# Optimization experiments

Measured on AMD Instinct MI355X. Metric: run time of the kernel, lower is better.

The kernel has to match this reference:

```python
import jax, jax.numpy as jnp
import numpy as np
import math

D_MODEL = 1024
N_HEADS = 16
HEAD_DIM = D_MODEL // N_HEADS


def get_slopes(n_heads: int) -> jnp.ndarray:
    def pow2_slopes(n):
        start = 2.0 ** (-8.0 / n)
        return np.array([start * start ** i for i in range(n)], dtype=np.float32)
    if math.log2(n_heads).is_integer():
        return jnp.asarray(pow2_slopes(n_heads))
    closest = 2 ** math.floor(math.log2(n_heads))
    base = pow2_slopes(closest)
    extra = pow2_slopes(2 * closest)[::2][: n_heads - closest]
    return jnp.asarray(np.concatenate([base, extra]))


def setup_inputs() -> dict:
    key = jax.random.key(0)
    ks = jax.random.split(key, 9)
    s = 1.0 / math.sqrt(D_MODEL)
    x = jax.random.normal(ks[0], (2, 2048, D_MODEL), dtype=jnp.float32)
    q_w = jax.random.uniform(ks[1], (D_MODEL, D_MODEL), jnp.float32, -s, s)
    q_b = jax.random.uniform(ks[2], (D_MODEL,), jnp.float32, -s, s)
    k_w = jax.random.uniform(ks[3], (D_MODEL, D_MODEL), jnp.float32, -s, s)
    k_b = jax.random.uniform(ks[4], (D_MODEL,), jnp.float32, -s, s)
    v_w = jax.random.uniform(ks[5], (D_MODEL, D_MODEL), jnp.float32, -s, s)
    v_b = jax.random.uniform(ks[6], (D_MODEL,), jnp.float32, -s, s)
    o_w = jax.random.uniform(ks[7], (D_MODEL, D_MODEL), jnp.float32, -s, s)
    o_b = jax.random.uniform(ks[8], (D_MODEL,), jnp.float32, -s, s)
    return {"x": x, "q_w": q_w, "q_b": q_b, "k_w": k_w, "k_b": k_b,
            "v_w": v_w, "v_b": v_b, "o_w": o_w, "o_b": o_b}


def reference(x, q_w, q_b, k_w, k_b, v_w, v_b, o_w, o_b):
    B, S, D = x.shape
    H, hd = N_HEADS, HEAD_DIM
    # torch Linear: y = x @ W.T + b
    Q = (x @ q_w.T + q_b).reshape(B, S, H, hd).transpose(0, 2, 1, 3)  # [B,H,S,hd]
    K = (x @ k_w.T + k_b).reshape(B, S, H, hd).transpose(0, 2, 1, 3)
    V = (x @ v_w.T + v_b).reshape(B, S, H, hd).transpose(0, 2, 1, 3)
    scores = jnp.einsum('bhqd,bhkd->bhqk', Q, K) / math.sqrt(hd)
    # ALiBi bias: slopes[h] * (k_pos - q_pos)
    pos = jnp.arange(S)
    rel = (pos[None, :] - pos[:, None]).astype(scores.dtype)  # [S,S]
    slopes = get_slopes(H)
    scores = scores + slopes[None, :, None, None] * rel[None, None, :, :]
    # causal mask
    causal = pos[None, :] <= pos[:, None]  # [S,S] True where allowed
    scores = jnp.where(causal[None, None], scores, -jnp.inf)
    attn = jax.nn.softmax(scores, axis=-1)  # dropout=0 (eval)
    out = jnp.einsum('bhqk,bhkd->bhqd', attn, V)
    out = out.transpose(0, 2, 1, 3).reshape(B, S, D)
    return out @ o_w.T + o_b
```

## Files before the change

### kernel.cpp

```cpp
#include <hip/hip_runtime.h>
#include <hip/hip_bf16.h>

typedef __attribute__((ext_vector_type(8))) short short8;
typedef __attribute__((ext_vector_type(4))) float float4v;
typedef __attribute__((ext_vector_type(4))) short short4v;
typedef __attribute__((ext_vector_type(4))) unsigned int uint4v;
typedef __attribute__((ext_vector_type(2))) unsigned int uint2v;

#define B_ 2
#define S_ 2048
#define D_ 1024
#define H_ 16
#define HD_ 64
#define M_ 4096
#define LOG2E 1.442695040888963f

__device__ __forceinline__ unsigned short f2bf(float f) {
  unsigned int u = __builtin_bit_cast(unsigned int, f);
  u += 0x7fffu + ((u >> 16) & 1u);
  return (unsigned short)(u >> 16);
}

__device__ __forceinline__ unsigned int pkbf(float a, float b) {
  __hip_bfloat162 h = __float22bfloat162_rn(make_float2(a, b));
  unsigned int u;
  __builtin_memcpy(&u, &h, sizeof(u));
  return u;
}

__device__ __forceinline__ void gload_lds16(const void* g, void* l) {
  __builtin_amdgcn_global_load_lds(
      (const __attribute__((address_space(1))) void*)g,
      (__attribute__((address_space(3))) void*)l, 16, 0, 0);
}

__global__ __launch_bounds__(256, 4) void cvt_kernel(
    const float* __restrict__ x,  const float* __restrict__ qw,
    const float* __restrict__ kw, const float* __restrict__ vw,
    const float* __restrict__ ow, unsigned short* __restrict__ dst)
{
  const int seg = blockIdx.y;
  const float* src;
  size_t doff;
  if (seg < 4)       { src = x + (size_t)seg * 1048576; doff = (size_t)seg * 1048576; }
  else if (seg == 4) { src = qw; doff = 4194304u; }
  else if (seg == 5) { src = kw; doff = 4194304u + 1048576u; }
  else if (seg == 6) { src = vw; doff = 4194304u + 2097152u; }
  else               { src = ow; doff = 4194304u + 3145728u; }
  const size_t i = ((size_t)blockIdx.x * 256 + threadIdx.x) * 4;
  float4v v = *(const float4v*)(src + i);
  short4v p;
#pragma unroll
  for (int r = 0; r < 4; ++r) p[r] = (short)f2bf(v[r]);
  *(short4v*)(dst + doff + i) = p;
}

__global__ __launch_bounds__(256, 2) void gemm_kernel(
    const unsigned short* __restrict__ X,
    const unsigned short* __restrict__ W0, const unsigned short* __restrict__ W1,
    const unsigned short* __restrict__ W2,
    const float* __restrict__ Bi0, const float* __restrict__ Bi1,
    const float* __restrict__ Bi2,
    unsigned short* O0, unsigned short* O1, unsigned short* O2,
    float* OutF, int md0, int md1, int md2)
{
  const int z = blockIdx.z;
  const unsigned short* W  = (z == 0) ? W0  : ((z == 1) ? W1  : W2);
  const float* Bi          = (z == 0) ? Bi0 : ((z == 1) ? Bi1 : Bi2);
  unsigned short* Out      = (z == 0) ? O0  : ((z == 1) ? O1  : O2);
  const int mode           = (z == 0) ? md0 : ((z == 1) ? md1 : md2);

  __shared__ __align__(16) char smem[128 * 32 * 2 * 2];
  __shared__ __align__(16) float tb[32 * 132];
  char* As = smem;
  char* Bs = smem + 128 * 32 * 2;

  const int t = threadIdx.x, l = t & 63;
  const int w = t >> 6, lr = l & 15, lg = l >> 4;
  const int n0 = blockIdx.x * 128, m0 = blockIdx.y * 128;
  const int wm = (w >> 1) * 64, wn = (w & 1) * 64;

  float4v acc[4][4];
#pragma unroll
  for (int i = 0; i < 4; ++i)
#pragma unroll
    for (int j = 0; j < 4; ++j) acc[i][j] = (float4v){0.f, 0.f, 0.f, 0.f};

  const int c0 = t, c1 = t + 256;
  const int r0 = c0 >> 2, k80 = (c0 & 3) * 8;
  const int r1 = c1 >> 2, k81 = (c1 & 3) * 8;

  for (int k0 = 0; k0 < 1024; k0 += 32) {
    __syncthreads();
    gload_lds16(X + (size_t)(m0 + r0) * 1024 + k0 + k80, As + c0 * 16);
    gload_lds16(X + (size_t)(m0 + r1) * 1024 + k0 + k81, As + c1 * 16);
    gload_lds16(W + (size_t)(n0 + r0) * 1024 + k0 + k80, Bs + c0 * 16);
    gload_lds16(W + (size_t)(n0 + r1) * 1024 + k0 + k81, Bs + c1 * 16);
    __syncthreads();

    short8 af[4], bfr[4];
#pragma unroll
    for (int i = 0; i < 4; ++i)
      af[i] = *(const short8*)(As + (wm + i * 16 + lr) * 64 + lg * 16);
#pragma unroll
    for (int j = 0; j < 4; ++j)
      bfr[j] = *(const short8*)(Bs + (wn + j * 16 + lr) * 64 + lg * 16);
#pragma unroll
    for (int i = 0; i < 4; ++i)
#pragma unroll
      for (int j = 0; j < 4; ++j)
        acc[i][j] = __builtin_amdgcn_mfma_f32_16x16x32_bf16(af[i], bfr[j], acc[i][j], 0, 0, 0);
  }

  float bv[4];
#pragma unroll
  for (int j = 0; j < 4; ++j) bv[j] = Bi[n0 + wn + j * 16 + lr];

  if (mode == 1) {
    const int rbase = (w >> 1) * 16;
    const int row16 = t >> 3, chunk = t & 7;
#pragma unroll
    for (int i = 0; i < 4; ++i) {
#pragma unroll
      for (int j = 0; j < 4; ++j)
#pragma unroll
        for (int r = 0; r < 4; ++r)
          tb[(rbase + lg * 4 + r) * 132 + wn + j * 16 + lr] = acc[i][j][r] + bv[j];
      __syncthreads();
      const int grow = m0 + ((row16 < 16) ? (i * 16 + row16) : (64 + i * 16 + row16 - 16));
      const int b = grow >> 11, sl = grow & 2047;
      const int colg = n0 + chunk * 16;
      const int hh = colg >> 6, d0 = colg & 63;
      float4v v4[4];
#pragma unroll
      for (int q = 0; q < 4; ++q)
        v4[q] = *(const float4v*)(tb + row16 * 132 + chunk * 16 + q * 4);
      uint4v lo, hi;
#pragma unroll
      for (int q = 0; q < 2; ++q) {
        lo[q * 2]     = pkbf(v4[q][0], v4[q][1]);
        lo[q * 2 + 1] = pkbf(v4[q][2], v4[q][3]);
        hi[q * 2]     = pkbf(v4[q + 2][0], v4[q + 2][1]);
        hi[q * 2 + 1] = pkbf(v4[q + 2][2], v4[q + 2][3]);
      }
      unsigned short* dst = Out + ((size_t)(b * H_ + hh) * S_ + sl) * HD_ + d0;
      *(short8*)dst = __builtin_bit_cast(short8, lo);
      *(short8*)(dst + 8) = __builtin_bit_cast(short8, hi);
      __syncthreads();
    }
  } else {
#pragma unroll
    for (int i = 0; i < 4; ++i) {
      const int rowb = m0 + wm + i * 16 + lg * 4;
#pragma unroll
      for (int j = 0; j < 4; ++j) {
        const int col = n0 + wn + j * 16 + lr;
        if (mode == 2) {
          const int b = rowb >> 11, s = rowb & 2047;
          const int hh = col >> 6, d = col & 63;
          uint2v pk2;
          pk2[0] = pkbf(acc[i][j][0] + bv[j], acc[i][j][1] + bv[j]);
          pk2[1] = pkbf(acc[i][j][2] + bv[j], acc[i][j][3] + bv[j]);
          *(short4v*)(Out + ((size_t)(b * H_ + hh) * HD_ + d) * S_ + s) =
              __builtin_bit_cast(short4v, pk2);
        } else {
#pragma unroll
          for (int r = 0; r < 4; ++r)
            OutF[(size_t)(rowb + r) * 1024 + col] = acc[i][j][r] + bv[j];
        }
      }
    }
  }
}

__global__ __launch_bounds__(256, 2) void attn_kernel(
    const unsigned short* __restrict__ Q, const unsigned short* __restrict__ K,
    const unsigned short* __restrict__ VT, unsigned short* __restrict__ O)
{
  __shared__ __align__(16) char smem[32768];

  const int t = threadIdx.x, l = t & 63;
  const int w = t >> 6, lr = l & 15, lg = l >> 4;
  const int bh = blockIdx.x;
  const int it = 31 - (int)blockIdx.y;
  const int h = bh & 15;

  const unsigned short* qbp = Q + (size_t)bh * S_ * HD_;
  const unsigned short* kbp = K + (size_t)bh * S_ * HD_;
  const unsigned short* vbp = VT + (size_t)bh * HD_ * S_;

  const float slope2 = __builtin_amdgcn_exp2f(-0.5f * (float)(h + 1)) * LOG2E;
  const float qksc = 0.125f * LOG2E;

  const int g0 = t, g1 = t + 256;
  const int sr0 = g0 >> 3, sc0 = (g0 & 7) ^ (sr0 & 7);
  const int sr1 = g1 >> 3, sc1 = (g1 & 7) ^ (sr1 & 7);

  const int fchunk = ((4 + lg) ^ (lr & 7)) * 16;
  const int fchunk0 = ((lg) ^ (lr & 7)) * 16;

  const int qrow = it * 64 + w * 16;
  const int qpos = qrow + lr;

  float kb16[4][4];
#pragma unroll
  for (int nj = 0; nj < 4; ++nj)
#pragma unroll
    for (int r = 0; r < 4; ++r)
      kb16[nj][r] = slope2 * (float)(nj * 16 + lg * 4 + r);

  short8 qf[2];
#pragma unroll
  for (int ks = 0; ks < 2; ++ks)
    qf[ks] = *(const short8*)(qbp + (size_t)(qrow + lr) * HD_ + ks * 32 + lg * 8);

  float4v o_acc[4];
#pragma unroll
  for (int dt = 0; dt < 4; ++dt) o_acc[dt] = (float4v){0.f, 0.f, 0.f, 0.f};
  float m_st = -1e30f, l_st = 0.f;

  gload_lds16(kbp + (size_t)sr0 * HD_ + sc0 * 8, smem + g0 * 16);
  gload_lds16(kbp + (size_t)sr1 * HD_ + sc1 * 8, smem + g1 * 16);
  gload_lds16(vbp + (size_t)sr0 * S_ + sc0 * 8, smem + 16384 + g0 * 16);
  gload_lds16(vbp + (size_t)sr1 * S_ + sc1 * 8, smem + 16384 + g1 * 16);
  __syncthreads();

  for (int j = 0; j <= it; ++j) {
    const int cur = j & 1;
    char* Ks = smem + (cur ? 8192 : 0);
    char* Vs = smem + 16384 + (cur ? 8192 : 0);
    if (j < it) {
      char* Kn = smem + (cur ? 0 : 8192);
      char* Vn = smem + 16384 + (cur ? 0 : 8192);
      const int jn = j + 1;
      gload_lds16(kbp + (size_t)(jn * 64 + sr0) * HD_ + sc0 * 8, Kn + g0 * 16);
      gload_lds16(kbp + (size_t)(jn * 64 + sr1) * HD_ + sc1 * 8, Kn + g1 * 16);
      gload_lds16(vbp + (size_t)sr0 * S_ + jn * 64 + sc0 * 8, Vn + g0 * 16);
      gload_lds16(vbp + (size_t)sr1 * S_ + jn * 64 + sc1 * 8, Vn + g1 * 16);
    }

    float4v s_acc[4];
#pragma unroll
    for (int nj = 0; nj < 4; ++nj) {
      s_acc[nj] = (float4v){0.f, 0.f, 0.f, 0.f};
      short8 kf0 = *(const short8*)(Ks + (nj * 16 + lr) * 128 + fchunk0);
      s_acc[nj] = __builtin_amdgcn_mfma_f32_16x16x32_bf16(kf0, qf[0], s_acc[nj], 0, 0, 0);
      short8 kf1 = *(const short8*)(Ks + (nj * 16 + lr) * 128 + fchunk);
      s_acc[nj] = __builtin_amdgcn_mfma_f32_16x16x32_bf16(kf1, qf[1], s_acc[nj], 0, 0, 0);
    }

    const float cj = slope2 * (float)(j * 64);
#pragma unroll
    for (int nj = 0; nj < 4; ++nj)
#pragma unroll
      for (int r = 0; r < 4; ++r)
        s_acc[nj][r] = s_acc[nj][r] * qksc + (cj + kb16[nj][r]);
    if (j == it) {
#pragma unroll
      for (int nj = 0; nj < 4; ++nj)
#pragma unroll
        for (int r = 0; r < 4; ++r) {
          const int kpos = j * 64 + nj * 16 + lg * 4 + r;
          if (kpos > qpos) s_acc[nj][r] = -1e30f;
        }
    }

    float mx = s_acc[0][0];
#pragma unroll
    for (int nj = 0; nj < 4; ++nj)
#pragma unroll
      for (int r = 0; r < 4; ++r) mx = fmaxf(mx, s_acc[nj][r]);
    mx = fmaxf(mx, __shfl_xor(mx, 16, 64));
    mx = fmaxf(mx, __shfl_xor(mx, 32, 64));
    const float mn = fmaxf(m_st, mx);
    const float alpha = __builtin_amdgcn_exp2f(m_st - mn);
    m_st = mn;
    float rsum = 0.f;
#pragma unroll
    for (int nj = 0; nj < 4; ++nj)
#pragma unroll
      for (int r = 0; r < 4; ++r) {
        const float p = __builtin_amdgcn_exp2f(s_acc[nj][r] - mn);
        s_acc[nj][r] = p;
        rsum += p;
      }
    rsum += __shfl_xor(rsum, 16, 64);
    rsum += __shfl_xor(rsum, 32, 64);
    l_st = alpha * l_st + rsum;
#pragma unroll
    for (int dt = 0; dt < 4; ++dt)
#pragma unroll
      for (int r = 0; r < 4; ++r) o_acc[dt][r] *= alpha;

    short8 pT[2];
#pragma unroll
    for (int njp = 0; njp < 2; ++njp) {
      uint4v u;
      u[0] = pkbf(s_acc[njp * 2][0], s_acc[njp * 2][1]);
      u[1] = pkbf(s_acc[njp * 2][2], s_acc[njp * 2][3]);
      u[2] = pkbf(s_acc[njp * 2 + 1][0], s_acc[njp * 2 + 1][1]);
      u[3] = pkbf(s_acc[njp * 2 + 1][2], s_acc[njp * 2 + 1][3]);
      pT[njp] = __builtin_bit_cast(short8, u);
    }

    const int vcl = lr & 7;
#pragma unroll
    for (int dt = 0; dt < 4; ++dt) {
      const char* rowp = Vs + (dt * 16 + lr) * 128;
#pragma unroll
      for (int njp = 0; njp < 2; ++njp) {
        const int cA = ((njp * 4 + (lg >> 1)) ^ vcl) * 16 + (lg & 1) * 8;
        const int cB = ((njp * 4 + 2 + (lg >> 1)) ^ vcl) * 16 + (lg & 1) * 8;
        short4v v0 = *(const short4v*)(rowp + cA);
        short4v v1 = *(const short4v*)(rowp + cB);
        short8 vf8;
#pragma unroll
        for (int e = 0; e < 4; ++e) { vf8[e] = v0[e]; vf8[e + 4] = v1[e]; }
        o_acc[dt] = __builtin_amdgcn_mfma_f32_16x16x32_bf16(vf8, pT[njp], o_acc[dt], 0, 0, 0);
      }
    }
    __syncthreads();
  }

  char* tw = smem + w * 4416;
#pragma unroll
  for (int dt = 0; dt < 4; ++dt)
#pragma unroll
    for (int r = 0; r < 4; ++r)
      *(float*)(tw + ((dt * 16 + lg * 4 + r) * 17 + lr) * 4) = o_acc[dt][r];
  if (lg == 0) *(float*)(tw + 4352 + lr * 4) = l_st;

  const int q2 = l >> 2, dbase = (l & 3) * 16;
  const float invl = 1.0f / *(const float*)(tw + 4352 + q2 * 4);
  uint4v os0, os1;
#pragma unroll
  for (int k = 0; k < 8; ++k) {
    const float va = *(const float*)(tw + ((dbase + 2 * k) * 17 + q2) * 4) * invl;
    const float vb = *(const float*)(tw + ((dbase + 2 * k + 1) * 17 + q2) * 4) * invl;
    if (k < 4) os0[k] = pkbf(va, vb); else os1[k - 4] = pkbf(va, vb);
  }
  const int brow = (bh >> 4) * S_;
  unsigned short* op = O + (size_t)(brow + qrow + q2) * 1024 + h * 64 + dbase;
  *(short8*)op = __builtin_bit_cast(short8, os0);
  *(short8*)(op + 8) = __builtin_bit_cast(short8, os1);
}

extern "C" void kernel_launch(void* const* d_in, const int* in_sizes, int n_in,
                              void* d_out, int out_size, void* d_ws, size_t ws_size,
                              hipStream_t stream) {
  (void)in_sizes; (void)n_in; (void)out_size; (void)ws_size;
  const float* x  = (const float*)d_in[0];
  const float* qw = (const float*)d_in[1];
  const float* qb = (const float*)d_in[2];
  const float* kw = (const float*)d_in[3];
  const float* kb = (const float*)d_in[4];
  const float* vw = (const float*)d_in[5];
  const float* vb = (const float*)d_in[6];
  const float* ow = (const float*)d_in[7];
  const float* ob = (const float*)d_in[8];
  float* out = (float*)d_out;

  unsigned short* xb  = (unsigned short*)d_ws;
  unsigned short* qwb = xb  + (size_t)M_ * D_;
  unsigned short* kwb = qwb + (size_t)D_ * D_;
  unsigned short* vwb = kwb + (size_t)D_ * D_;
  unsigned short* owb = vwb + (size_t)D_ * D_;
  unsigned short* qws = owb + (size_t)D_ * D_;
  unsigned short* kws = qws + (size_t)M_ * D_;
  unsigned short* vws = kws + (size_t)M_ * D_;
  unsigned short* aws = vws + (size_t)M_ * D_;

  cvt_kernel<<<dim3(1024, 8), dim3(256), 0, stream>>>(x, qw, kw, vw, ow, xb);
  gemm_kernel<<<dim3(8, 32, 3), dim3(256), 0, stream>>>(
      xb, qwb, kwb, vwb, qb, kb, vb, qws, kws, vws, out, 1, 1, 2);
  attn_kernel<<<dim3(32, 32), dim3(256), 0, stream>>>(qws, kws, vws, aws);
  gemm_kernel<<<dim3(8, 32, 1), dim3(256), 0, stream>>>(
      aws, owb, owb, owb, ob, ob, ob, aws, aws, aws, out, 0, 0, 0);
}
```

Before: 194.4 us.

## Use narrower output-projection GEMM tiles and compute softmax row sums via MFMA

Templates the GEMM on the N tile width and launches the output projection with 64-wide tiles, doubling block count from 256 to 512 so more CUs are filled. In attention, the softmax denominator is accumulated by an MFMA against a ones vector over the bf16 probabilities, replacing per-lane adds and cross-lane shuffles. ALiBi offsets are now computed inline, freeing 16 precomputed registers. The sum now uses bf16-rounded probabilities, which matches what multiplies V but changes rounding slightly.

```diff
diff --git a/kernel.cpp b/kernel.cpp
--- a/kernel.cpp
+++ b/kernel.cpp
@@ -55,6 +55,7 @@
   *(short4v*)(dst + doff + i) = p;
 }
 
+template <int TN>
 __global__ __launch_bounds__(256, 2) void gemm_kernel(
     const unsigned short* __restrict__ X,
     const unsigned short* __restrict__ W0, const unsigned short* __restrict__ W1,
@@ -64,27 +65,28 @@
     unsigned short* O0, unsigned short* O1, unsigned short* O2,
     float* OutF, int md0, int md1, int md2)
 {
+  constexpr int NJ = TN / 32;
   const int z = blockIdx.z;
   const unsigned short* W  = (z == 0) ? W0  : ((z == 1) ? W1  : W2);
   const float* Bi          = (z == 0) ? Bi0 : ((z == 1) ? Bi1 : Bi2);
   unsigned short* Out      = (z == 0) ? O0  : ((z == 1) ? O1  : O2);
   const int mode           = (z == 0) ? md0 : ((z == 1) ? md1 : md2);
 
-  __shared__ __align__(16) char smem[128 * 32 * 2 * 2];
+  __shared__ __align__(16) char smem[8192 + TN * 64];
   __shared__ __align__(16) float tb[32 * 132];
   char* As = smem;
-  char* Bs = smem + 128 * 32 * 2;
+  char* Bs = smem + 8192;
 
   const int t = threadIdx.x, l = t & 63;
   const int w = t >> 6, lr = l & 15, lg = l >> 4;
-  const int n0 = blockIdx.x * 128, m0 = blockIdx.y * 128;
-  const int wm = (w >> 1) * 64, wn = (w & 1) * 64;
-
-  float4v acc[4][4];
+  const int n0 = blockIdx.x * TN, m0 = blockIdx.y * 128;
+  const int wm = (w >> 1) * 64, wn = (w & 1) * (TN / 2);
+
+  float4v acc[4][NJ];
 #pragma unroll
   for (int i = 0; i < 4; ++i)
 #pragma unroll
-    for (int j = 0; j < 4; ++j) acc[i][j] = (float4v){0.f, 0.f, 0.f, 0.f};
+    for (int j = 0; j < NJ; ++j) acc[i][j] = (float4v){0.f, 0.f, 0.f, 0.f};
 
   const int c0 = t, c1 = t + 256;
   const int r0 = c0 >> 2, k80 = (c0 & 3) * 8;
@@ -95,67 +97,70 @@
     gload_lds16(X + (size_t)(m0 + r0) * 1024 + k0 + k80, As + c0 * 16);
     gload_lds16(X + (size_t)(m0 + r1) * 1024 + k0 + k81, As + c1 * 16);
     gload_lds16(W + (size_t)(n0 + r0) * 1024 + k0 + k80, Bs + c0 * 16);
-    gload_lds16(W + (size_t)(n0 + r1) * 1024 + k0 + k81, Bs + c1 * 16);
+    if (TN == 128)
+      gload_lds16(W + (size_t)(n0 + r1) * 1024 + k0 + k81, Bs + c1 * 16);
     __syncthreads();
 
-    short8 af[4], bfr[4];
+    short8 af[4], bfr[NJ];
 #pragma unroll
     for (int i = 0; i < 4; ++i)
       af[i] = *(const short8*)(As + (wm + i * 16 + lr) * 64 + lg * 16);
 #pragma unroll
-    for (int j = 0; j < 4; ++j)
+    for (int j = 0; j < NJ; ++j)
       bfr[j] = *(const short8*)(Bs + (wn + j * 16 + lr) * 64 + lg * 16);
 #pragma unroll
     for (int i = 0; i < 4; ++i)
 #pragma unroll
-      for (int j = 0; j < 4; ++j)
+      for (int j = 0; j < NJ; ++j)
         acc[i][j] = __builtin_amdgcn_mfma_f32_16x16x32_bf16(af[i], bfr[j], acc[i][j], 0, 0, 0);
   }
 
-  float bv[4];
-#pragma unroll
-  for (int j = 0; j < 4; ++j) bv[j] = Bi[n0 + wn + j * 16 + lr];
-
-  if (mode == 1) {
-    const int rbase = (w >> 1) * 16;
-    const int row16 = t >> 3, chunk = t & 7;
-#pragma unroll
-    for (int i = 0; i < 4; ++i) {
-#pragma unroll
-      for (int j = 0; j < 4; ++j)
-#pragma unroll
-        for (int r = 0; r < 4; ++r)
-          tb[(rbase + lg * 4 + r) * 132 + wn + j * 16 + lr] = acc[i][j][r] + bv[j];
-      __syncthreads();
-      const int grow = m0 + ((row16 < 16) ? (i * 16 + row16) : (64 + i * 16 + row16 - 16));
-      const int b = grow >> 11, sl = grow & 2047;
-      const int colg = n0 + chunk * 16;
-      const int hh = colg >> 6, d0 = colg & 63;
-      float4v v4[4];
-#pragma unroll
-      for (int q = 0; q < 4; ++q)
-        v4[q] = *(const float4v*)(tb + row16 * 132 + chunk * 16 + q * 4);
-      uint4v lo, hi;
-#pragma unroll
-      for (int q = 0; q < 2; ++q) {
-        lo[q * 2]     = pkbf(v4[q][0], v4[q][1]);
-        lo[q * 2 + 1] = pkbf(v4[q][2], v4[q][3]);
-        hi[q * 2]     = pkbf(v4[q + 2][0], v4[q + 2][1]);
-        hi[q * 2 + 1] = pkbf(v4[q + 2][2], v4[q + 2][3]);
+  float bv[NJ];
+#pragma unroll
+  for (int j = 0; j < NJ; ++j) bv[j] = Bi[n0 + wn + j * 16 + lr];
+
+  if constexpr (TN == 128) {
+    if (mode == 1) {
+      const int rbase = (w >> 1) * 16;
+      const int row16 = t >> 3, chunk = t & 7;
+#pragma unroll
+      for (int i = 0; i < 4; ++i) {
+#pragma unroll
+        for (int j = 0; j < 4; ++j)
+#pragma unroll
+          for (int r = 0; r < 4; ++r)
+            tb[(rbase + lg * 4 + r) * 132 + wn + j * 16 + lr] = acc[i][j][r] + bv[j];
+        __syncthreads();
+        const int grow = m0 + ((row16 < 16) ? (i * 16 + row16) : (64 + i * 16 + row16 - 16));
+        const int b = grow >> 11, sl = grow & 2047;
+        const int colg = n0 + chunk * 16;
+        const int hh = colg >> 6, d0 = colg & 63;
+        float4v v4[4];
+#pragma unroll
+        for (int q = 0; q < 4; ++q)
+          v4[q] = *(const float4v*)(tb + row16 * 132 + chunk * 16 + q * 4);
+        uint4v lo, hi;
+#pragma unroll
+        for (int q = 0; q < 2; ++q) {
+          lo[q * 2]     = pkbf(v4[q][0], v4[q][1]);
+          lo[q * 2 + 1] = pkbf(v4[q][2], v4[q][3]);
+          hi[q * 2]     = pkbf(v4[q + 2][0], v4[q + 2][1]);
+          hi[q * 2 + 1] = pkbf(v4[q + 2][2], v4[q + 2][3]);
+        }
+        unsigned short* dst = Out + ((size_t)(b * H_ + hh) * S_ + sl) * HD_ + d0;
+        *(short8*)dst = __builtin_bit_cast(short8, lo);
+        *(short8*)(dst + 8) = __builtin_bit_cast(short8, hi);
+        __syncthreads();
       }
-      unsigned short* dst = Out + ((size_t)(b * H_ + hh) * S_ + sl) * HD_ + d0;
-      *(short8*)dst = __builtin_bit_cast(short8, lo);
-      *(short8*)(dst + 8) = __builtin_bit_cast(short8, hi);
-      __syncthreads();
-    }
-  } else {
-#pragma unroll
-    for (int i = 0; i < 4; ++i) {
-      const int rowb = m0 + wm + i * 16 + lg * 4;
-#pragma unroll
-      for (int j = 0; j < 4; ++j) {
-        const int col = n0 + wn + j * 16 + lr;
-        if (mode == 2) {
+      return;
+    }
+    if (mode == 2) {
+#pragma unroll
+      for (int i = 0; i < 4; ++i) {
+        const int rowb = m0 + wm + i * 16 + lg * 4;
+#pragma unroll
+        for (int j = 0; j < 4; ++j) {
+          const int col = n0 + wn + j * 16 + lr;
           const int b = rowb >> 11, s = rowb & 2047;
           const int hh = col >> 6, d = col & 63;
           uint2v pk2;
@@ -163,12 +168,20 @@
           pk2[1] = pkbf(acc[i][j][2] + bv[j], acc[i][j][3] + bv[j]);
           *(short4v*)(Out + ((size_t)(b * H_ + hh) * HD_ + d) * S_ + s) =
               __builtin_bit_cast(short4v, pk2);
-        } else {
-#pragma unroll
-          for (int r = 0; r < 4; ++r)
-            OutF[(size_t)(rowb + r) * 1024 + col] = acc[i][j][r] + bv[j];
         }
       }
+      return;
+    }
+  }
+#pragma unroll
+  for (int i = 0; i < 4; ++i) {
+    const int rowb = m0 + wm + i * 16 + lg * 4;
+#pragma unroll
+    for (int j = 0; j < NJ; ++j) {
+      const int col = n0 + wn + j * 16 + lr;
+#pragma unroll
+      for (int r = 0; r < 4; ++r)
+        OutF[(size_t)(rowb + r) * 1024 + col] = acc[i][j][r] + bv[j];
     }
   }
 }
@@ -202,22 +215,20 @@
   const int qrow = it * 64 + w * 16;
   const int qpos = qrow + lr;
 
-  float kb16[4][4];
-#pragma unroll
-  for (int nj = 0; nj < 4; ++nj)
-#pragma unroll
-    for (int r = 0; r < 4; ++r)
-      kb16[nj][r] = slope2 * (float)(nj * 16 + lg * 4 + r);
+  short8 ones;
+#pragma unroll
+  for (int e = 0; e < 8; ++e) ones[e] = (short)0x3F80;
 
   short8 qf[2];
 #pragma unroll
   for (int ks = 0; ks < 2; ++ks)
     qf[ks] = *(const short8*)(qbp + (size_t)(qrow + lr) * HD_ + ks * 32 + lg * 8);
 
-  float4v o_acc[4];
+  float4v o_acc[4], l_acc;
 #pragma unroll
   for (int dt = 0; dt < 4; ++dt) o_acc[dt] = (float4v){0.f, 0.f, 0.f, 0.f};
-  float m_st = -1e30f, l_st = 0.f;
+  l_acc = (float4v){0.f, 0.f, 0.f, 0.f};
+  float m_st = -1e30f;
 
   gload_lds16(kbp + (size_t)sr0 * HD_ + sc0 * 8, smem + g0 * 16);
   gload_lds16(kbp + (size_t)sr1 * HD_ + sc1 * 8, smem + g1 * 16);
@@ -249,12 +260,13 @@
       s_acc[nj] = __builtin_amdgcn_mfma_f32_16x16x32_bf16(kf1, qf[1], s_acc[nj], 0, 0, 0);
     }
 
-    const float cj = slope2 * (float)(j * 64);
-#pragma unroll
-    for (int nj = 0; nj < 4; ++nj)
+#pragma unroll
+    for (int nj = 0; nj < 4; ++nj) {
+      const float cb = slope2 * (float)(j * 64 + nj * 16 + lg * 4);
 #pragma unroll
       for (int r = 0; r < 4; ++r)
-        s_acc[nj][r] = s_acc[nj][r] * qksc + (cj + kb16[nj][r]);
+        s_acc[nj][r] = s_acc[nj][r] * qksc + (cb + slope2 * (float)r);
+    }
     if (j == it) {
 #pragma unroll
       for (int nj = 0; nj < 4; ++nj)
@@ -275,22 +287,17 @@
     const float mn = fmaxf(m_st, mx);
     const float alpha = __builtin_amdgcn_exp2f(m_st - mn);
     m_st = mn;
-    float rsum = 0.f;
 #pragma unroll
     for (int nj = 0; nj < 4; ++nj)
 #pragma unroll
-      for (int r = 0; r < 4; ++r) {
-        const float p = __builtin_amdgcn_exp2f(s_acc[nj][r] - mn);
-        s_acc[nj][r] = p;
-        rsum += p;
-      }
-    rsum += __shfl_xor(rsum, 16, 64);
-    rsum += __shfl_xor(rsum, 32, 64);
-    l_st = alpha * l_st + rsum;
+      for (int r = 0; r < 4; ++r)
+        s_acc[nj][r] = __builtin_amdgcn_exp2f(s_acc[nj][r] - mn);
 #pragma unroll
     for (int dt = 0; dt < 4; ++dt)
 #pragma unroll
       for (int r = 0; r < 4; ++r) o_acc[dt][r] *= alpha;
+#pragma unroll
+    for (int r = 0; r < 4; ++r) l_acc[r] *= alpha;
 
     short8 pT[2];
 #pragma unroll
@@ -303,6 +310,9 @@
       pT[njp] = __builtin_bit_cast(short8, u);
     }
 
+    l_acc = __builtin_amdgcn_mfma_f32_16x16x32_bf16(ones, pT[0], l_acc, 0, 0, 0);
+    l_acc = __builtin_amdgcn_mfma_f32_16x16x32_bf16(ones, pT[1], l_acc, 0, 0, 0);
+
     const int vcl = lr & 7;
 #pragma unroll
     for (int dt = 0; dt < 4; ++dt) {
@@ -328,7 +338,7 @@
 #pragma unroll
     for (int r = 0; r < 4; ++r)
       *(float*)(tw + ((dt * 16 + lg * 4 + r) * 17 + lr) * 4) = o_acc[dt][r];
-  if (lg == 0) *(float*)(tw + 4352 + lr * 4) = l_st;
+  if (lg == 0) *(float*)(tw + 4352 + lr * 4) = l_acc[0];
 
   const int q2 = l >> 2, dbase = (l & 3) * 16;
   const float invl = 1.0f / *(const float*)(tw + 4352 + q2 * 4);
@@ -371,9 +381,9 @@
   unsigned short* aws = vws + (size_t)M_ * D_;
 
   cvt_kernel<<<dim3(1024, 8), dim3(256), 0, stream>>>(x, qw, kw, vw, ow, xb);
-  gemm_kernel<<<dim3(8, 32, 3), dim3(256), 0, stream>>>(
+  gemm_kernel<128><<<dim3(8, 32, 3), dim3(256), 0, stream>>>(
       xb, qwb, kwb, vwb, qb, kb, vb, qws, kws, vws, out, 1, 1, 2);
   attn_kernel<<<dim3(32, 32), dim3(256), 0, stream>>>(qws, kws, vws, aws);
-  gemm_kernel<<<dim3(8, 32, 1), dim3(256), 0, stream>>>(
+  gemm_kernel<64><<<dim3(16, 32, 1), dim3(256), 0, stream>>>(
       aws, owb, owb, owb, ob, ob, ob, aws, aws, aws, out, 0, 0, 0);
 }
```

Result: faster. 186.4 us (-4.1%).
